# Kernel optimization log

Hardware: AMD Instinct MI355X
Metric: run time of the kernel (lower is better)

Reference implementation:

```python
import jax, jax.numpy as jnp
import numpy as np

ROPE_THETA = 10000.0
N_KV_HEADS = 8


def _rope(x, pos, theta):
    # x: [..., D] with interleaved (even, odd) rotation pairs; pos: scalar position
    D = x.shape[-1]
    freqs = theta ** (-jnp.arange(0, D, 2, dtype=jnp.float32) / D)  # [D/2]
    ang = pos * freqs
    cos, sin = jnp.cos(ang), jnp.sin(ang)
    x1, x2 = x[..., 0::2], x[..., 1::2]
    return jnp.stack([x1 * cos - x2 * sin, x1 * sin + x2 * cos], axis=-1).reshape(x.shape)


def setup_inputs() -> dict:
    key = jax.random.key(0)
    ks = jax.random.split(key, 5)
    B, DIM, CACHE_LEN, HD = 32, 4096, 4096, 128
    N_HEADS = 32
    qkv_out = (N_HEADS + 2 * N_KV_HEADS) * HD  # 6144
    return {
        "x": jax.random.normal(ks[0], (B, DIM), dtype=jnp.float32),
        "cache_k": jax.random.normal(ks[1], (B, CACHE_LEN, N_KV_HEADS, HD), dtype=jnp.float32),
        "cache_v": jax.random.normal(ks[2], (B, CACHE_LEN, N_KV_HEADS, HD), dtype=jnp.float32),
        "wqkv": jax.random.normal(ks[3], (qkv_out, DIM), dtype=jnp.float32) * 0.02,
        "wo": jax.random.normal(ks[4], (DIM, DIM), dtype=jnp.float32) * 0.02,
        "ctx_len": 4095,
    }


def reference(x, cache_k, cache_v, wqkv, wo, ctx_len):
    B = x.shape[0]
    n_kv = cache_k.shape[2]
    hd = cache_k.shape[3]
    n_heads = (wqkv.shape[0] - 2 * n_kv * hd) // hd
    hpg = n_heads // n_kv  # heads per kv group

    # fused QKV projection
    xqkv = x @ wqkv.T  # [B, (n_heads + 2*n_kv)*hd]
    nq = n_heads * hd
    nk = n_kv * hd
    q = xqkv[:, :nq].reshape(B, n_kv, hpg, hd)
    k = xqkv[:, nq:nq + nk].reshape(B, n_kv, hd)
    v = xqkv[:, nq + nk:].reshape(B, n_kv, hd)

    # rope fused with KV-cache write: new token at position ctx_len
    q = _rope(q, ctx_len, ROPE_THETA)
    k = _rope(k, ctx_len, ROPE_THETA)
    cache_k = cache_k.at[:, ctx_len].set(k)
    cache_v = cache_v.at[:, ctx_len].set(v)

    T = ctx_len + 1  # valid cache length (python int -> static slice)
    K = cache_k[:, :T]  # [B, T, n_kv, hd]
    V = cache_v[:, :T]

    # GQA attention: q [b, g, h, d], K/V [b, t, g, d]
    scores = jnp.einsum("bghd,btgd->bght", q, K) / jnp.sqrt(jnp.float32(hd))
    w = jax.nn.softmax(scores, axis=-1)
    o = jnp.einsum("bght,btgd->bghd", w, V).reshape(B, n_heads * hd)
    return o @ wo.T
```

## Files before the change

### kernel.cpp

```cpp
#include <hip/hip_runtime.h>
#include <math.h>

#define BATCH 32
#define DIM   4096
#define CLEN  4096
#define HD    128
#define NKV   8
#define NHEAD 32
#define QKVN  6144
#define KVSTR (NKV * HD)
#define GN    64
#define KSEG  128
#define KSTG  4
#define KTOT  512
#define NSEG  8
#define NCHB  16
#define TC    256
#define NSLOT 16
#define MNEG  -1.0e30f
#define SMASK -3.0e38f

template <int CTRL>
__device__ __forceinline__ float dpp_add(float x) {
  int y = __builtin_amdgcn_update_dpp(0, __float_as_int(x), CTRL, 0xF, 0xF, true);
  return x + __int_as_float(y);
}

__device__ __forceinline__ float half_reduce(float s) {
  s = dpp_add<0xB1>(s);
  s = dpp_add<0x4E>(s);
  s = dpp_add<0x124>(s);
  s = dpp_add<0x128>(s);
  s += __int_as_float(__builtin_amdgcn_ds_swizzle(__float_as_int(s), 0x401F));
  return s;
}

__global__ __launch_bounds__(256)
void gemm_partial(const float* __restrict__ X, const float* __restrict__ W,
                  float* __restrict__ part, const int N) {
  __shared__ float xs[KSEG * 32];
  __shared__ float wl[KSEG * 64];
  const int tid = threadIdx.x;
  const int c   = tid & 31;
  const int r   = tid >> 5;
  const int cx7 = c & 7;
  const int n0  = blockIdx.x * GN;
  const int k00 = blockIdx.y * KTOT;
  const int bq8 = tid & 7;
  const int tq  = tid >> 3;
  const int nqq = tq >> 1;
  const int nqo = (tq & 1) << 1;

  float a00=0,a01=0, a10=0,a11=0, a20=0,a21=0, a30=0,a31=0;

  float* xwp  = xs + (c * 4) * 32 + ((r ^ cx7) << 2);
  float* wwp0 = wl + (c * 4) * 64 + ((r ^ cx7) << 2);
  float* wwp1 = wwp0 + 32;

  float4 xv0, xv1, xv2, xv3, wv00, wv01, wv02, wv03, wv10, wv11, wv12, wv13;
  {
    const float* Xp = X + (size_t)(r * 4) * DIM + k00 + c * 4;
    xv0 = *(const float4*)(Xp);
    xv1 = *(const float4*)(Xp + DIM);
    xv2 = *(const float4*)(Xp + 2 * DIM);
    xv3 = *(const float4*)(Xp + 3 * DIM);
    const float* Wp0 = W + (size_t)(n0 + r * 4) * DIM + k00 + c * 4;
    wv00 = *(const float4*)(Wp0);
    wv01 = *(const float4*)(Wp0 + DIM);
    wv02 = *(const float4*)(Wp0 + 2 * DIM);
    wv03 = *(const float4*)(Wp0 + 3 * DIM);
    const float* Wp1 = Wp0 + (size_t)32 * DIM;
    wv10 = *(const float4*)(Wp1);
    wv11 = *(const float4*)(Wp1 + DIM);
    wv12 = *(const float4*)(Wp1 + 2 * DIM);
    wv13 = *(const float4*)(Wp1 + 3 * DIM);
  }

  for (int kk = 0; kk < KSTG; ++kk) {
    if (kk) __syncthreads();

    *(float4*)(xwp + 0)   = make_float4(xv0.x, xv1.x, xv2.x, xv3.x);
    *(float4*)(xwp + 32)  = make_float4(xv0.y, xv1.y, xv2.y, xv3.y);
    *(float4*)(xwp + 64)  = make_float4(xv0.z, xv1.z, xv2.z, xv3.z);
    *(float4*)(xwp + 96)  = make_float4(xv0.w, xv1.w, xv2.w, xv3.w);
    *(float4*)(wwp0 + 0)   = make_float4(wv00.x, wv01.x, wv02.x, wv03.x);
    *(float4*)(wwp0 + 64)  = make_float4(wv00.y, wv01.y, wv02.y, wv03.y);
    *(float4*)(wwp0 + 128) = make_float4(wv00.z, wv01.z, wv02.z, wv03.z);
    *(float4*)(wwp0 + 192) = make_float4(wv00.w, wv01.w, wv02.w, wv03.w);
    *(float4*)(wwp1 + 0)   = make_float4(wv10.x, wv11.x, wv12.x, wv13.x);
    *(float4*)(wwp1 + 64)  = make_float4(wv10.y, wv11.y, wv12.y, wv13.y);
    *(float4*)(wwp1 + 128) = make_float4(wv10.z, wv11.z, wv12.z, wv13.z);
    *(float4*)(wwp1 + 192) = make_float4(wv10.w, wv11.w, wv12.w, wv13.w);
    __syncthreads();

    if (kk + 1 < KSTG) {
      const int k0 = k00 + (kk + 1) * KSEG;
      const float* Xp = X + (size_t)(r * 4) * DIM + k0 + c * 4;
      xv0 = *(const float4*)(Xp);
      xv1 = *(const float4*)(Xp + DIM);
      xv2 = *(const float4*)(Xp + 2 * DIM);
      xv3 = *(const float4*)(Xp + 3 * DIM);
      const float* Wp0 = W + (size_t)(n0 + r * 4) * DIM + k0 + c * 4;
      wv00 = *(const float4*)(Wp0);
      wv01 = *(const float4*)(Wp0 + DIM);
      wv02 = *(const float4*)(Wp0 + 2 * DIM);
      wv03 = *(const float4*)(Wp0 + 3 * DIM);
      const float* Wp1 = Wp0 + (size_t)32 * DIM;
      wv10 = *(const float4*)(Wp1);
      wv11 = *(const float4*)(Wp1 + DIM);
      wv12 = *(const float4*)(Wp1 + 2 * DIM);
      wv13 = *(const float4*)(Wp1 + 3 * DIM);
    }

#pragma unroll 8
    for (int k2 = 0; k2 < KSEG / 4; ++k2) {
      const int g = k2 & 7;
      const float* xr = xs + (k2 * 4) * 32 + ((bq8 ^ g) << 2);
      const float* wr = wl + (k2 * 4) * 64 + ((nqq ^ g) << 2) + nqo;
#pragma unroll
      for (int j = 0; j < 4; ++j) {
        const float4 xv = *(const float4*)(xr + j * 32);
        const float2 wv = *(const float2*)(wr + j * 64);
        a00 = fmaf(xv.x, wv.x, a00); a01 = fmaf(xv.x, wv.y, a01);
        a10 = fmaf(xv.y, wv.x, a10); a11 = fmaf(xv.y, wv.y, a11);
        a20 = fmaf(xv.z, wv.x, a20); a21 = fmaf(xv.z, wv.y, a21);
        a30 = fmaf(xv.w, wv.x, a30); a31 = fmaf(xv.w, wv.y, a31);
      }
    }
  }
  const int bq = bq8 << 2;
  const int nq = tq << 1;
  float* base = part + ((size_t)blockIdx.y * BATCH + bq) * N + n0 + nq;
  *(float2*)(base)         = make_float2(a00, a01);
  *(float2*)(base + N)     = make_float2(a10, a11);
  *(float2*)(base + 2 * N) = make_float2(a20, a21);
  *(float2*)(base + 3 * N) = make_float2(a30, a31);
}

__global__ __launch_bounds__(256)
void qkv_combine(const float* __restrict__ part, const int* __restrict__ ctxp,
                 float* __restrict__ qw, float* __restrict__ kn, float* __restrict__ vn) {
  const int idx = blockIdx.x * 256 + threadIdx.x;
  const int b  = idx / (QKVN / 2);
  const int c  = idx % (QKVN / 2);
  const int n0 = c * 2;
  float v0 = 0.f, v1 = 0.f;
#pragma unroll
  for (int s = 0; s < NSEG; ++s) {
    const float2 pv = *(const float2*)(part + ((size_t)s * BATCH + b) * QKVN + n0);
    v0 += pv.x; v1 += pv.y;
  }
  const float pos = (float)ctxp[0];
  const float L2T_OVER_64 = 0.20762050593045952f;
  if (n0 < DIM) {
    const int i = (n0 & 127) >> 1;
    const float fr = exp2f(-(float)i * L2T_OVER_64);
    float sn, cs; sincosf(pos * fr, &sn, &cs);
    qw[(size_t)b * DIM + n0]     = v0 * cs - v1 * sn;
    qw[(size_t)b * DIM + n0 + 1] = v0 * sn + v1 * cs;
  } else if (n0 < DIM + NKV * HD) {
    const int nk = n0 - DIM;
    const int i = (nk & 127) >> 1;
    const float fr = exp2f(-(float)i * L2T_OVER_64);
    float sn, cs; sincosf(pos * fr, &sn, &cs);
    kn[(size_t)b * (NKV * HD) + nk]     = v0 * cs - v1 * sn;
    kn[(size_t)b * (NKV * HD) + nk + 1] = v0 * sn + v1 * cs;
  } else {
    const int nv = n0 - DIM - NKV * HD;
    vn[(size_t)b * (NKV * HD) + nv]     = v0;
    vn[(size_t)b * (NKV * HD) + nv + 1] = v1;
  }
}

__device__ __forceinline__ void load4(float4 kb[4], float4 vb[4],
    const float* __restrict__ kbase, const float* __restrict__ vbase,
    const float* __restrict__ knr, const float* __restrict__ vnr,
    const int t0, const int ctx, const bool edge) {
#pragma unroll
  for (int u = 0; u < 4; ++u) {
    const int row = t0 + u;
    const float* kp = kbase + (size_t)row * KVSTR;
    const float* vp = vbase + (size_t)row * KVSTR;
    if (edge) {
      if (row == ctx) { kp = knr; vp = vnr; }
    }
    kb[u] = *(const float4*)kp;
    vb[u] = *(const float4*)vp;
  }
}

__device__ __forceinline__ void compute4(const float4 kb[4], const float4 vb[4],
    const float4 q[4], const int t0, const int ctx, const bool edge,
    float m[4], float l[4], float4 acc[4]) {
#pragma unroll
  for (int u = 0; u < 4; ++u) {
    float s[4];
#pragma unroll
    for (int hh = 0; hh < 4; ++hh) {
      float d = fmaf(kb[u].x, q[hh].x, kb[u].y * q[hh].y);
      d = fmaf(kb[u].z, q[hh].z, d);
      d = fmaf(kb[u].w, q[hh].w, d);
      s[hh] = half_reduce(d);
    }
    if (edge) {
      if (t0 + u > ctx) { s[0] = SMASK; s[1] = SMASK; s[2] = SMASK; s[3] = SMASK; }
    }
    if ((s[0] > m[0]) | (s[1] > m[1]) | (s[2] > m[2]) | (s[3] > m[3])) {
#pragma unroll
      for (int hh = 0; hh < 4; ++hh) {
        const float mn = fmaxf(m[hh], s[hh]);
        const float rs = __expf(m[hh] - mn);
        l[hh] *= rs;
        acc[hh].x *= rs; acc[hh].y *= rs; acc[hh].z *= rs; acc[hh].w *= rs;
        m[hh] = mn;
      }
    }
#pragma unroll
    for (int hh = 0; hh < 4; ++hh) {
      const float p = __expf(s[hh] - m[hh]);
      l[hh] += p;
      acc[hh].x = fmaf(p, vb[u].x, acc[hh].x);
      acc[hh].y = fmaf(p, vb[u].y, acc[hh].y);
      acc[hh].z = fmaf(p, vb[u].z, acc[hh].z);
      acc[hh].w = fmaf(p, vb[u].w, acc[hh].w);
    }
  }
}

__global__ __launch_bounds__(256)
void attn_fd(const float* __restrict__ qw, const float* __restrict__ knew,
             const float* __restrict__ vnew, const float* __restrict__ ck,
             const float* __restrict__ cv, const int* __restrict__ ctxp,
             float* __restrict__ opart, float* __restrict__ mlp) {
  const int b    = blockIdx.x >> 4;
  const int cidx = blockIdx.x & (NCHB - 1);
  const int wid  = threadIdx.x >> 6;
  const int lane = threadIdx.x & 63;
  const int half = lane >> 5;
  const int g    = wid * 2 + half;
  const int d4   = (lane & 31) << 2;
  const int ctx  = ctxp[0];
  const int c0   = cidx * TC;

  const float sc = 0.08838834764831845f;
  float4 q[4];
#pragma unroll
  for (int hh = 0; hh < 4; ++hh) {
    q[hh] = *(const float4*)(qw + ((size_t)b * NHEAD + g * 4 + hh) * HD + d4);
    q[hh].x *= sc; q[hh].y *= sc; q[hh].z *= sc; q[hh].w *= sc;
  }
  const float* kbase = ck + ((size_t)b * CLEN) * KVSTR + g * HD + d4;
  const float* vbase = cv + ((size_t)b * CLEN) * KVSTR + g * HD + d4;
  const float* knr   = knew + ((size_t)b * NKV + g) * HD + d4;
  const float* vnr   = vnew + ((size_t)b * NKV + g) * HD + d4;

  float m[4] = {MNEG, MNEG, MNEG, MNEG};
  float l[4] = {0.f, 0.f, 0.f, 0.f};
  float4 acc[4] = {};

  float4 kA[4], vA[4], kB[4], vB[4];
  load4(kA, vA, kbase, vbase, knr, vnr, c0, ctx, c0 + 4 > ctx);
  for (int it = 0; it < TC / 8; ++it) {
    const int t0 = c0 + it * 8;
    load4(kB, vB, kbase, vbase, knr, vnr, t0 + 4, ctx, t0 + 8 > ctx);
    compute4(kA, vA, q, t0, ctx, t0 + 4 > ctx, m, l, acc);
    if (it + 1 < TC / 8)
      load4(kA, vA, kbase, vbase, knr, vnr, t0 + 8, ctx, t0 + 12 > ctx);
    compute4(kB, vB, q, t0 + 4, ctx, t0 + 8 > ctx, m, l, acc);
  }

#pragma unroll
  for (int hh = 0; hh < 4; ++hh) {
    const int hid = b * NHEAD + g * 4 + hh;
    const size_t slot = (size_t)hid * NSLOT + cidx;
    *(float4*)(opart + slot * HD + d4) = acc[hh];
    if ((lane & 31) == 0) { mlp[slot * 2] = m[hh]; mlp[slot * 2 + 1] = l[hh]; }
  }
}

__global__ __launch_bounds__(128)
void attn_combine(const float* __restrict__ opart, const float* __restrict__ mlp,
                  float* __restrict__ ow) {
  const int p = blockIdx.x;
  const int d = threadIdx.x;
  float M = MNEG;
#pragma unroll
  for (int c = 0; c < NSLOT; ++c) M = fmaxf(M, mlp[((size_t)p * NSLOT + c) * 2]);
  float L = 0.f, O = 0.f;
#pragma unroll 8
  for (int c = 0; c < NSLOT; ++c) {
    const float mi = mlp[((size_t)p * NSLOT + c) * 2];
    const float w = __expf(mi - M);
    L += w * mlp[((size_t)p * NSLOT + c) * 2 + 1];
    O += w * opart[((size_t)p * NSLOT + c) * HD + d];
  }
  ow[(size_t)p * HD + d] = O / L;
}

__global__ __launch_bounds__(256)
void sum_partials(const float* __restrict__ part, float* __restrict__ out,
                  const int total4, const int nseg, const int stride) {
  const int i = blockIdx.x * 256 + threadIdx.x;
  if (i >= total4) return;
  float4 s = make_float4(0.f, 0.f, 0.f, 0.f);
  for (int g = 0; g < nseg; ++g) {
    const float4 v = *(const float4*)(part + (size_t)g * stride + (size_t)i * 4);
    s.x += v.x; s.y += v.y; s.z += v.z; s.w += v.w;
  }
  *(float4*)(out + (size_t)i * 4) = s;
}

extern "C" void kernel_launch(void* const* d_in, const int* in_sizes, int n_in,
                              void* d_out, int out_size, void* d_ws, size_t ws_size,
                              hipStream_t stream) {
  const float* x    = (const float*)d_in[0];
  const float* ck   = (const float*)d_in[1];
  const float* cv   = (const float*)d_in[2];
  const float* wqkv = (const float*)d_in[3];
  const float* wo   = (const float*)d_in[4];
  const int*   ctx  = (const int*)d_in[5];

  float* ws    = (float*)d_ws;
  float* pqkv  = ws;
  float* qw    = pqkv + (size_t)NSEG * BATCH * QKVN;
  float* kn    = qw + (size_t)BATCH * DIM;
  float* vn    = kn + (size_t)BATCH * NKV * HD;
  float* opart = vn + (size_t)BATCH * NKV * HD;
  float* mlp   = opart + (size_t)1024 * NSLOT * HD;
  float* ow    = mlp + (size_t)1024 * NSLOT * 2;
  float* pout  = pqkv;

  gemm_partial<<<dim3(QKVN / GN, NSEG), 256, 0, stream>>>(x, wqkv, pqkv, QKVN);
  qkv_combine<<<dim3(BATCH * QKVN / 2 / 256), 256, 0, stream>>>(pqkv, ctx, qw, kn, vn);
  attn_fd<<<dim3(BATCH * NCHB), 256, 0, stream>>>(qw, kn, vn, ck, cv, ctx, opart, mlp);
  attn_combine<<<dim3(BATCH * NHEAD), HD, 0, stream>>>(opart, mlp, ow);
  gemm_partial<<<dim3(DIM / GN, NSEG), 256, 0, stream>>>(ow, wo, pout, DIM);
  sum_partials<<<dim3((BATCH * DIM / 4 + 255) / 256), 256, 0, stream>>>(
      pout, (float*)d_out, BATCH * DIM / 4, NSEG, BATCH * DIM);
}
```

Baseline: 276.5 us.

## Stage GEMM tiles with direct global-to-LDS loads and double buffering

```diff
diff --git a/kernel.cpp b/kernel.cpp
--- a/kernel.cpp
+++ b/kernel.cpp
@@ -20,6 +20,12 @@
 #define MNEG  -1.0e30f
 #define SMASK -3.0e38f
 
+__device__ __forceinline__ void gload_lds16(const float* g, float* l) {
+  __builtin_amdgcn_global_load_lds(
+      (const __attribute__((address_space(1))) void*)g,
+      (__attribute__((address_space(3))) void*)l, 16, 0, 0);
+}
+
 template <int CTRL>
 __device__ __forceinline__ float dpp_add(float x) {
   int y = __builtin_amdgcn_update_dpp(0, __float_as_int(x), CTRL, 0xF, 0xF, true);
@@ -38,99 +44,68 @@
 __global__ __launch_bounds__(256)
 void gemm_partial(const float* __restrict__ X, const float* __restrict__ W,
                   float* __restrict__ part, const int N) {
-  __shared__ float xs[KSEG * 32];
-  __shared__ float wl[KSEG * 64];
-  const int tid = threadIdx.x;
-  const int c   = tid & 31;
-  const int r   = tid >> 5;
-  const int cx7 = c & 7;
-  const int n0  = blockIdx.x * GN;
-  const int k00 = blockIdx.y * KTOT;
-  const int bq8 = tid & 7;
-  const int tq  = tid >> 3;
-  const int nqq = tq >> 1;
-  const int nqo = (tq & 1) << 1;
+  __shared__ float xs[2][BATCH * KSEG];
+  __shared__ float wl[2][GN * KSEG];
+  const int tid  = threadIdx.x;
+  const int wid  = tid >> 6;
+  const int kqst = tid & 31;
+  const int rsub = tid >> 5;
+  const int n0   = blockIdx.x * GN;
+  const int k00  = blockIdx.y * KTOT;
+  const int bsel = tid & 7;
+  const int tsel = tid >> 3;
+  const int bq4  = bsel << 2;
+  const int nq   = tsel << 1;
 
   float a00=0,a01=0, a10=0,a11=0, a20=0,a21=0, a30=0,a31=0;
 
-  float* xwp  = xs + (c * 4) * 32 + ((r ^ cx7) << 2);
-  float* wwp0 = wl + (c * 4) * 64 + ((r ^ cx7) << 2);
-  float* wwp1 = wwp0 + 32;
-
-  float4 xv0, xv1, xv2, xv3, wv00, wv01, wv02, wv03, wv10, wv11, wv12, wv13;
-  {
-    const float* Xp = X + (size_t)(r * 4) * DIM + k00 + c * 4;
-    xv0 = *(const float4*)(Xp);
-    xv1 = *(const float4*)(Xp + DIM);
-    xv2 = *(const float4*)(Xp + 2 * DIM);
-    xv3 = *(const float4*)(Xp + 3 * DIM);
-    const float* Wp0 = W + (size_t)(n0 + r * 4) * DIM + k00 + c * 4;
-    wv00 = *(const float4*)(Wp0);
-    wv01 = *(const float4*)(Wp0 + DIM);
-    wv02 = *(const float4*)(Wp0 + 2 * DIM);
-    wv03 = *(const float4*)(Wp0 + 3 * DIM);
-    const float* Wp1 = Wp0 + (size_t)32 * DIM;
-    wv10 = *(const float4*)(Wp1);
-    wv11 = *(const float4*)(Wp1 + DIM);
-    wv12 = *(const float4*)(Wp1 + 2 * DIM);
-    wv13 = *(const float4*)(Wp1 + 3 * DIM);
-  }
-
+  auto stage = [&](int buf, int k0) {
+#pragma unroll
+    for (int i = 0; i < 4; ++i) {
+      const int row = i * 8 + rsub;
+      const int sx  = (row >> 2) & 7;
+      gload_lds16(X + (size_t)row * DIM + k0 + 4 * (kqst ^ sx),
+                  &xs[buf][(i * 8 + wid * 2) * KSEG]);
+    }
+#pragma unroll
+    for (int j = 0; j < 8; ++j) {
+      const int row = j * 8 + rsub;
+      const int sw  = (row >> 1) & 7;
+      gload_lds16(W + (size_t)(n0 + row) * DIM + k0 + 4 * (kqst ^ sw),
+                  &wl[buf][(j * 8 + wid * 2) * KSEG]);
+    }
+  };
+
+  stage(0, k00);
+  __syncthreads();
+  int buf = 0;
   for (int kk = 0; kk < KSTG; ++kk) {
-    if (kk) __syncthreads();
-
-    *(float4*)(xwp + 0)   = make_float4(xv0.x, xv1.x, xv2.x, xv3.x);
-    *(float4*)(xwp + 32)  = make_float4(xv0.y, xv1.y, xv2.y, xv3.y);
-    *(float4*)(xwp + 64)  = make_float4(xv0.z, xv1.z, xv2.z, xv3.z);
-    *(float4*)(xwp + 96)  = make_float4(xv0.w, xv1.w, xv2.w, xv3.w);
-    *(float4*)(wwp0 + 0)   = make_float4(wv00.x, wv01.x, wv02.x, wv03.x);
-    *(float4*)(wwp0 + 64)  = make_float4(wv00.y, wv01.y, wv02.y, wv03.y);
-    *(float4*)(wwp0 + 128) = make_float4(wv00.z, wv01.z, wv02.z, wv03.z);
-    *(float4*)(wwp0 + 192) = make_float4(wv00.w, wv01.w, wv02.w, wv03.w);
-    *(float4*)(wwp1 + 0)   = make_float4(wv10.x, wv11.x, wv12.x, wv13.x);
-    *(float4*)(wwp1 + 64)  = make_float4(wv10.y, wv11.y, wv12.y, wv13.y);
-    *(float4*)(wwp1 + 128) = make_float4(wv10.z, wv11.z, wv12.z, wv13.z);
-    *(float4*)(wwp1 + 192) = make_float4(wv10.w, wv11.w, wv12.w, wv13.w);
+    if (kk + 1 < KSTG) stage(buf ^ 1, k00 + (kk + 1) * KSEG);
+    const float* xb = &xs[buf][0];
+    const float* wb = &wl[buf][0];
+#pragma unroll 8
+    for (int kq = 0; kq < 32; ++kq) {
+      const int xo = 4 * (kq ^ bsel);
+      const int wo = 4 * (kq ^ (tsel & 7));
+      const float4 x0 = *(const float4*)(xb + (bq4 + 0) * KSEG + xo);
+      const float4 x1 = *(const float4*)(xb + (bq4 + 1) * KSEG + xo);
+      const float4 x2 = *(const float4*)(xb + (bq4 + 2) * KSEG + xo);
+      const float4 x3 = *(const float4*)(xb + (bq4 + 3) * KSEG + xo);
+      const float4 w0 = *(const float4*)(wb + (nq + 0) * KSEG + wo);
+      const float4 w1 = *(const float4*)(wb + (nq + 1) * KSEG + wo);
+      a00 = fmaf(x0.x,w0.x,a00); a00 = fmaf(x0.y,w0.y,a00); a00 = fmaf(x0.z,w0.z,a00); a00 = fmaf(x0.w,w0.w,a00);
+      a01 = fmaf(x0.x,w1.x,a01); a01 = fmaf(x0.y,w1.y,a01); a01 = fmaf(x0.z,w1.z,a01); a01 = fmaf(x0.w,w1.w,a01);
+      a10 = fmaf(x1.x,w0.x,a10); a10 = fmaf(x1.y,w0.y,a10); a10 = fmaf(x1.z,w0.z,a10); a10 = fmaf(x1.w,w0.w,a10);
+      a11 = fmaf(x1.x,w1.x,a11); a11 = fmaf(x1.y,w1.y,a11); a11 = fmaf(x1.z,w1.z,a11); a11 = fmaf(x1.w,w1.w,a11);
+      a20 = fmaf(x2.x,w0.x,a20); a20 = fmaf(x2.y,w0.y,a20); a20 = fmaf(x2.z,w0.z,a20); a20 = fmaf(x2.w,w0.w,a20);
+      a21 = fmaf(x2.x,w1.x,a21); a21 = fmaf(x2.y,w1.y,a21); a21 = fmaf(x2.z,w1.z,a21); a21 = fmaf(x2.w,w1.w,a21);
+      a30 = fmaf(x3.x,w0.x,a30); a30 = fmaf(x3.y,w0.y,a30); a30 = fmaf(x3.z,w0.z,a30); a30 = fmaf(x3.w,w0.w,a30);
+      a31 = fmaf(x3.x,w1.x,a31); a31 = fmaf(x3.y,w1.y,a31); a31 = fmaf(x3.z,w1.z,a31); a31 = fmaf(x3.w,w1.w,a31);
+    }
     __syncthreads();
-
-    if (kk + 1 < KSTG) {
-      const int k0 = k00 + (kk + 1) * KSEG;
-      const float* Xp = X + (size_t)(r * 4) * DIM + k0 + c * 4;
-      xv0 = *(const float4*)(Xp);
-      xv1 = *(const float4*)(Xp + DIM);
-      xv2 = *(const float4*)(Xp + 2 * DIM);
-      xv3 = *(const float4*)(Xp + 3 * DIM);
-      const float* Wp0 = W + (size_t)(n0 + r * 4) * DIM + k0 + c * 4;
-      wv00 = *(const float4*)(Wp0);
-      wv01 = *(const float4*)(Wp0 + DIM);
-      wv02 = *(const float4*)(Wp0 + 2 * DIM);
-      wv03 = *(const float4*)(Wp0 + 3 * DIM);
-      const float* Wp1 = Wp0 + (size_t)32 * DIM;
-      wv10 = *(const float4*)(Wp1);
-      wv11 = *(const float4*)(Wp1 + DIM);
-      wv12 = *(const float4*)(Wp1 + 2 * DIM);
-      wv13 = *(const float4*)(Wp1 + 3 * DIM);
-    }
-
-#pragma unroll 8
-    for (int k2 = 0; k2 < KSEG / 4; ++k2) {
-      const int g = k2 & 7;
-      const float* xr = xs + (k2 * 4) * 32 + ((bq8 ^ g) << 2);
-      const float* wr = wl + (k2 * 4) * 64 + ((nqq ^ g) << 2) + nqo;
-#pragma unroll
-      for (int j = 0; j < 4; ++j) {
-        const float4 xv = *(const float4*)(xr + j * 32);
-        const float2 wv = *(const float2*)(wr + j * 64);
-        a00 = fmaf(xv.x, wv.x, a00); a01 = fmaf(xv.x, wv.y, a01);
-        a10 = fmaf(xv.y, wv.x, a10); a11 = fmaf(xv.y, wv.y, a11);
-        a20 = fmaf(xv.z, wv.x, a20); a21 = fmaf(xv.z, wv.y, a21);
-        a30 = fmaf(xv.w, wv.x, a30); a31 = fmaf(xv.w, wv.y, a31);
-      }
-    }
-  }
-  const int bq = bq8 << 2;
-  const int nq = tq << 1;
-  float* base = part + ((size_t)blockIdx.y * BATCH + bq) * N + n0 + nq;
+    buf ^= 1;
+  }
+  float* base = part + ((size_t)blockIdx.y * BATCH + bq4) * N + n0 + nq;
   *(float2*)(base)         = make_float2(a00, a01);
   *(float2*)(base + N)     = make_float2(a10, a11);
   *(float2*)(base + 2 * N) = make_float2(a20, a21);
```

Result: slower. 302.3 us (+9.3%).
